# Performance work log

Hardware: AMD Instinct MI355X
Metric: run time of the kernel (lower is better)

The kernel has to match this reference:

```python
import jax, jax.numpy as jnp
import numpy as np

WIN = (2, 4, 4)
SHIFT = (1, 2, 2)
NUM_HEADS = 8
LN_EPS = 1e-5


def _rel_pos_index(ws):
    wt, wh, ww = ws
    coords = np.stack(np.meshgrid(np.arange(wt), np.arange(wh), np.arange(ww), indexing='ij'))
    cf = coords.reshape(3, -1)                      # [3, N]
    rel = cf[:, :, None] - cf[:, None, :]           # [3, N, N]
    rel = rel.transpose(1, 2, 0).copy()             # [N, N, 3]
    rel[..., 0] += wt - 1
    rel[..., 1] += wh - 1
    rel[..., 2] += ww - 1
    rel[..., 0] *= (2 * wh - 1) * (2 * ww - 1)
    rel[..., 1] *= 2 * ww - 1
    return rel.sum(-1)                              # [N, N] int

REL_IDX = _rel_pos_index(WIN)


def _layer_norm(x, w, b):
    mu = jnp.mean(x, axis=-1, keepdims=True)
    var = jnp.mean(jnp.square(x - mu), axis=-1, keepdims=True)
    return (x - mu) * jax.lax.rsqrt(var + LN_EPS) * w + b


def setup_inputs() -> dict:
    key = jax.random.key(0)
    ks = jax.random.split(key, 8)
    C, Cm = 256, 1024
    inp = {
        'x': jax.random.normal(ks[0], (2, 16, 64, 64, C), jnp.float32),
        'norm1_w': jnp.ones((C,), jnp.float32),
        'norm1_b': jnp.zeros((C,), jnp.float32),
        'qkv_w': jax.random.normal(ks[1], (C, 3 * C), jnp.float32) * 0.02,
        'qkv_b': jnp.zeros((3 * C,), jnp.float32),
        'proj_w': jax.random.normal(ks[2], (C, C), jnp.float32) * 0.02,
        'proj_b': jnp.zeros((C,), jnp.float32),
        'rel_bias_table': jax.random.normal(ks[3], (147, NUM_HEADS), jnp.float32) * 0.02,
        'norm2_w': jnp.ones((C,), jnp.float32),
        'norm2_b': jnp.zeros((C,), jnp.float32),
        'mlp_w1': jax.random.normal(ks[4], (C, Cm), jnp.float32) * 0.02,
        'mlp_b1': jnp.zeros((Cm,), jnp.float32),
        'mlp_w2': jax.random.normal(ks[5], (Cm, C), jnp.float32) * 0.02,
        'mlp_b2': jnp.zeros((C,), jnp.float32),
    }
    return inp


def reference(x, norm1_w, norm1_b, qkv_w, qkv_b, proj_w, proj_b,
              rel_bias_table, norm2_w, norm2_b, mlp_w1, mlp_b1, mlp_w2, mlp_b2):
    B, T, H, W, C = x.shape
    wT, wH, wW = WIN
    nh = NUM_HEADS
    d = C // nh
    scale = d ** (-0.5)
    N = wT * wH * wW

    shortcut = x
    h = _layer_norm(x, norm1_w, norm1_b)
    # cyclic shift (no attention mask is applied in the original block)
    h = jnp.roll(h, shift=(-SHIFT[0], -SHIFT[1], -SHIFT[2]), axis=(1, 2, 3))
    # window partition -> [B*nW, N, C]
    h = h.reshape(B, T // wT, wT, H // wH, wH, W // wW, wW, C)
    h = h.transpose(0, 1, 3, 5, 2, 4, 6, 7).reshape(-1, N, C)
    B_ = h.shape[0]

    qkv = (h @ qkv_w + qkv_b).reshape(B_, N, 3, nh, d).transpose(2, 0, 3, 1, 4)
    q, k, v = qkv[0] * scale, qkv[1], qkv[2]          # [B_, nh, N, d]
    attn = jnp.einsum('bhnd,bhmd->bhnm', q, k)        # [B_, nh, N, N]
    bias = rel_bias_table[REL_IDX].transpose(2, 0, 1)  # [nh, N, N]
    attn = jax.nn.softmax(attn + bias[None], axis=-1)
    o = jnp.einsum('bhnm,bhmd->bhnd', attn, v)
    o = o.transpose(0, 2, 1, 3).reshape(B_, N, C)
    o = o @ proj_w + proj_b

    # window reverse -> [B, T, H, W, C]
    o = o.reshape(B, T // wT, H // wH, W // wW, wT, wH, wW, C)
    o = o.transpose(0, 1, 4, 2, 5, 3, 6, 7).reshape(B, T, H, W, C)
    o = jnp.roll(o, shift=SHIFT, axis=(1, 2, 3))

    x = shortcut + o
    m = _layer_norm(x, norm2_w, norm2_b)
    m = jax.nn.gelu(m @ mlp_w1 + mlp_b1, approximate=False) @ mlp_w2 + mlp_b2
    return x + m
```

## Files before the change

kernel.cpp:

```cpp
#include <hip/hip_runtime.h>
#include <hip/hip_bf16.h>
#include <cstdint>
#include <cstddef>

typedef __attribute__((ext_vector_type(8)))  short  s16x8;
typedef __attribute__((ext_vector_type(4)))  float  fp32x4;
typedef __attribute__((ext_vector_type(16))) float  fp32x16;
typedef __attribute__((ext_vector_type(4)))  unsigned short u16x4;

static __device__ __forceinline__ float bf2f(unsigned short u) {
    union { unsigned int i; float f; } v; v.i = ((unsigned int)u) << 16; return v.f;
}
static __device__ __forceinline__ unsigned short f2bf(float f) {
    __hip_bfloat16 h = __float2bfloat16(f);
    return __builtin_bit_cast(unsigned short, h);
}

static __device__ __forceinline__ fp32x16 mfma32(s16x8 a, s16x8 b, fp32x16 c) {
    return __builtin_amdgcn_mfma_f32_32x32x16_bf16(a, b, c, 0, 0, 0);
}
static __device__ __forceinline__ fp32x4 mfma16(s16x8 a, s16x8 b, fp32x4 c) {
    return __builtin_amdgcn_mfma_f32_16x16x32_bf16(a, b, c, 0, 0, 0);
}

static __device__ __forceinline__ float wave_sum(float v) {
#pragma unroll
    for (int off = 32; off > 0; off >>= 1) v += __shfl_xor(v, off, 64);
    return v;
}

#define NTOK   131072
#define CDIM   256

__global__ void prep_kernel(const float* __restrict__ qkv_w, const float* __restrict__ proj_w,
                            const float* __restrict__ w1,    const float* __restrict__ w2,
                            const float* __restrict__ rel,
                            unsigned short* __restrict__ qkvT, unsigned short* __restrict__ projT,
                            unsigned short* __restrict__ w1T,  unsigned short* __restrict__ w2T,
                            float* __restrict__ btab) {
    int id = blockIdx.x * 256 + threadIdx.x;
    if (id < 196608) {
        int n = id >> 8, k = id & 255;
        qkvT[id] = f2bf(qkv_w[k * 768 + n]);
    } else if (id < 262144) {
        int e = id - 196608; int n = e >> 8, k = e & 255;
        projT[e] = f2bf(proj_w[k * 256 + n]);
    } else if (id < 524288) {
        int e = id - 262144; int n = e >> 8, k = e & 255;
        w1T[e] = f2bf(w1[k * 1024 + n]);
    } else if (id < 786432) {
        int e = id - 524288; int n = e >> 10, k = e & 1023;
        w2T[e] = f2bf(w2[k * 256 + n]);
    } else {
        int e = id - 786432;
        int h = e >> 10, rem = e & 1023, n = rem >> 5, m = rem & 31;
        int tn = n >> 4, hn = (n >> 2) & 3, wn = n & 3;
        int tm = m >> 4, hm = (m >> 2) & 3, wm = m & 3;
        int ridx = (tn - tm + 1) * 49 + (hn - hm + 3) * 7 + (wn - wm + 3);
        btab[e] = rel[ridx * 8 + h];
    }
}

template <int MODE>
__global__ __launch_bounds__(256) void ln_kernel(const float* __restrict__ in,
                                                 const float* __restrict__ w,
                                                 const float* __restrict__ b,
                                                 unsigned short* __restrict__ out) {
    int tid = threadIdx.x, lane = tid & 63, wid = tid >> 6;
    long r = (long)blockIdx.x * 4 + wid;
    long src;
    if (MODE == 0) {
        int n = (int)(r & 31); int win = (int)(r >> 5);
        int b_ = win >> 11, tw = (win >> 8) & 7, hw = (win >> 4) & 15, ww = win & 15;
        int ti = n >> 4, hi = (n >> 2) & 3, wi = n & 3;
        int t = tw * 2 + ti, hh = hw * 4 + hi, wv = ww * 4 + wi;
        int ts = (t + 1) & 15, hs = (hh + 2) & 63, wsd = (wv + 2) & 63;
        src = ((long)((b_ * 16 + ts) * 64 + hs)) * 64 + wsd;
    } else {
        src = r;
    }
    float4 v = *(const float4*)&in[src * CDIM + lane * 4];
    float vv[4] = {v.x, v.y, v.z, v.w};
    float s = vv[0] + vv[1] + vv[2] + vv[3];
    s = wave_sum(s);
    float mean = s * (1.0f / 256.0f);
    float q = vv[0]*vv[0] + vv[1]*vv[1] + vv[2]*vv[2] + vv[3]*vv[3];
    q = wave_sum(q);
    float var = q * (1.0f / 256.0f) - mean * mean;
    float rstd = rsqrtf(var + 1e-5f);
    int c0 = lane * 4;
    u16x4 o;
#pragma unroll
    for (int j = 0; j < 4; ++j)
        o[j] = f2bf((vv[j] - mean) * rstd * w[c0 + j] + b[c0 + j]);
    *(u16x4*)&out[r * CDIM + c0] = o;
}

template <int K, int EPI, int NS>
__global__ __launch_bounds__(256, 2) void gemm_k(const unsigned short* __restrict__ A,
                                                 const unsigned short* __restrict__ Bt,
                                                 const float* __restrict__ bias,
                                                 float* __restrict__ outf,
                                                 unsigned short* __restrict__ outb,
                                                 const float* __restrict__ resid) {
    __shared__ unsigned short smem[32768];
    const int tid = threadIdx.x;
    const int lane = tid & 63, wid = tid >> 6;
    const int m0 = blockIdx.y * 128, n0 = blockIdx.x * 128;
    const int wm = (wid >> 1) * 64, wn = (wid & 1) * 64;
    constexpr int NK = K / 64;

    fp32x4 acc[4][4] = {};

    auto stage = [&](int kt, int buf) {
#pragma unroll
        for (int i = 0; i < 4; ++i) {
            int L = i * 256 + tid;
            int r = L >> 3, c = L & 7;
            int sw = c ^ (r & 7);
            const unsigned short* ga = A + (size_t)(m0 + r) * K + kt * 64 + sw * 8;
            __builtin_amdgcn_global_load_lds(
                (const __attribute__((address_space(1))) void*)ga,
                (__attribute__((address_space(3))) void*)(smem + buf * 16384 + L * 8),
                16, 0, 0);
            const unsigned short* gb = Bt + (size_t)(n0 + r) * K + kt * 64 + sw * 8;
            __builtin_amdgcn_global_load_lds(
                (const __attribute__((address_space(1))) void*)gb,
                (__attribute__((address_space(3))) void*)(smem + buf * 16384 + 8192 + L * 8),
                16, 0, 0);
        }
    };

    stage(0, 0);
    for (int kt = 0; kt < NK; ++kt) {
        __syncthreads();
        if (kt + 1 < NK) stage(kt + 1, (kt + 1) & 1);
        const unsigned short* As = smem + (kt & 1) * 16384;
        const unsigned short* Bs = As + 8192;
#pragma unroll
        for (int ks = 0; ks < 2; ++ks) {
            s16x8 a[4], b[4];
#pragma unroll
            for (int m = 0; m < 4; ++m) {
                int row = wm + m * 16 + (lane & 15);
                int ch = (ks * 4 + (lane >> 4)) ^ (row & 7);
                a[m] = *(const s16x8*)(As + row * 64 + ch * 8);
            }
#pragma unroll
            for (int n = 0; n < 4; ++n) {
                int row = wn + n * 16 + (lane & 15);
                int ch = (ks * 4 + (lane >> 4)) ^ (row & 7);
                b[n] = *(const s16x8*)(Bs + row * 64 + ch * 8);
            }
#pragma unroll
            for (int m = 0; m < 4; ++m)
#pragma unroll
                for (int n = 0; n < 4; ++n)
                    acc[m][n] = mfma16(a[m], b[n], acc[m][n]);
        }
    }

    float bv[4];
#pragma unroll
    for (int n = 0; n < 4; ++n) bv[n] = bias[n0 + wn + n * 16 + (lane & 15)];

#pragma unroll
    for (int m = 0; m < 4; ++m) {
#pragma unroll
        for (int rg = 0; rg < 4; ++rg) {
            int row_t = wm + m * 16 + ((lane >> 4) << 2) + rg;
            size_t gr = (size_t)m0 + row_t;
            size_t dst = 0;
            if (EPI == 1) {
                int win = (int)(gr >> 5), n_ = (int)(gr & 31);
                int b_ = win >> 11, tw = (win >> 8) & 7, hw = (win >> 4) & 15, ww = win & 15;
                int ti = n_ >> 4, hi = (n_ >> 2) & 3, wi = n_ & 3;
                int t = tw * 2 + ti, hh = hw * 4 + hi, wv = ww * 4 + wi;
                int ts = (t + 1) & 15, hs = (hh + 2) & 63, wsd = (wv + 2) & 63;
                dst = ((size_t)((b_ * 16 + ts) * 64 + hs)) * 64 + wsd;
            }
#pragma unroll
            for (int n = 0; n < 4; ++n) {
                int gc = n0 + wn + n * 16 + (lane & 15);
                float v = acc[m][n][rg] + bv[n];
                if (EPI == 0) {
                    outb[gr * NS + gc] = f2bf(v);
                } else if (EPI == 1) {
                    outf[dst * CDIM + gc] = resid[dst * CDIM + gc] + v;
                } else if (EPI == 2) {
                    float g = 0.5f * v * (1.0f + erff(v * 0.70710678118654752f));
                    outb[gr * NS + gc] = f2bf(g);
                } else {
                    outf[gr * NS + gc] += v;
                }
            }
        }
    }
}

__global__ __launch_bounds__(256) void attn_kernel(const unsigned short* __restrict__ qkv,
                                                   const float* __restrict__ btab,
                                                   unsigned short* __restrict__ obuf) {
    __shared__ unsigned short sP[4][1280];
    __shared__ unsigned short sVt[4][1280];
    int tid = threadIdx.x, lane = tid & 63, wid = tid >> 6;
    int task = blockIdx.x * 4 + wid;
    int win = task >> 3, hh = task & 7;
    const unsigned short* base = qkv + (size_t)win * 32 * 768 + hh * 32;
    int q = lane & 31, h = lane >> 5;

    s16x8 v0 = *(const s16x8*)(base + 512 + q * 768 + h * 16);
    s16x8 v1 = *(const s16x8*)(base + 512 + q * 768 + h * 16 + 8);
#pragma unroll
    for (int j = 0; j < 8; ++j) {
        sVt[wid][(h * 16 + j) * 40 + q]     = (unsigned short)v0[j];
        sVt[wid][(h * 16 + 8 + j) * 40 + q] = (unsigned short)v1[j];
    }

    s16x8 aq0 = *(const s16x8*)(base + q * 768 + h * 8);
    s16x8 aq1 = *(const s16x8*)(base + q * 768 + 16 + h * 8);
    s16x8 bk0 = *(const s16x8*)(base + 256 + q * 768 + h * 8);
    s16x8 bk1 = *(const s16x8*)(base + 256 + q * 768 + 16 + h * 8);
    fp32x16 S = {0.0f};
    S = mfma32(aq0, bk0, S);
    S = mfma32(aq1, bk1, S);

    const float scale = 0.17677669529663687f;
    float pr[16];
#pragma unroll
    for (int r = 0; r < 16; ++r) {
        int row = (r & 3) + 8 * (r >> 2) + 4 * h;
        float bvv = btab[(hh * 32 + row) * 32 + q];
        pr[r] = S[r] * scale + bvv;
    }
#pragma unroll
    for (int r = 0; r < 16; ++r) {
        float mx = pr[r];
#pragma unroll
        for (int off = 16; off > 0; off >>= 1) mx = fmaxf(mx, __shfl_xor(mx, off, 64));
        float e = __expf(pr[r] - mx);
        float sm = e;
#pragma unroll
        for (int off = 16; off > 0; off >>= 1) sm += __shfl_xor(sm, off, 64);
        pr[r] = e * __builtin_amdgcn_rcpf(sm);
    }
#pragma unroll
    for (int r = 0; r < 16; ++r) {
        int row = (r & 3) + 8 * (r >> 2) + 4 * h;
        sP[wid][row * 40 + q] = f2bf(pr[r]);
    }
    __syncthreads();

    s16x8 pa0 = *(const s16x8*)&sP[wid][q * 40 + h * 8];
    s16x8 pa1 = *(const s16x8*)&sP[wid][q * 40 + 16 + h * 8];
    s16x8 vb0 = *(const s16x8*)&sVt[wid][q * 40 + h * 8];
    s16x8 vb1 = *(const s16x8*)&sVt[wid][q * 40 + 16 + h * 8];
    fp32x16 O = {0.0f};
    O = mfma32(pa0, vb0, O);
    O = mfma32(pa1, vb1, O);
#pragma unroll
    for (int r = 0; r < 16; ++r) {
        int row = (r & 3) + 8 * (r >> 2) + 4 * h;
        obuf[((size_t)win * 32 + row) * 256 + hh * 32 + q] = f2bf(O[r]);
    }
}

extern "C" void kernel_launch(void* const* d_in, const int* in_sizes, int n_in,
                              void* d_out, int out_size, void* d_ws, size_t ws_size,
                              hipStream_t stream) {
    const float* x      = (const float*)d_in[0];
    const float* n1w    = (const float*)d_in[1];
    const float* n1b    = (const float*)d_in[2];
    const float* qkv_w  = (const float*)d_in[3];
    const float* qkv_b  = (const float*)d_in[4];
    const float* proj_w = (const float*)d_in[5];
    const float* proj_b = (const float*)d_in[6];
    const float* rel    = (const float*)d_in[7];
    const float* n2w    = (const float*)d_in[8];
    const float* n2b    = (const float*)d_in[9];
    const float* w1     = (const float*)d_in[10];
    const float* b1     = (const float*)d_in[11];
    const float* w2     = (const float*)d_in[12];
    const float* b2     = (const float*)d_in[13];
    float* out = (float*)d_out;

    char* ws = (char*)d_ws;
    unsigned short* hwin = (unsigned short*)ws;
    unsigned short* big  = (unsigned short*)(ws + 67108864);
    char* wreg = ws + 67108864 + 268435456;
    unsigned short* qkvT  = (unsigned short*)(wreg);
    unsigned short* projT = (unsigned short*)(wreg + 393216);
    unsigned short* w1T   = (unsigned short*)(wreg + 524288);
    unsigned short* w2T   = (unsigned short*)(wreg + 1048576);
    float*          btab  = (float*)(wreg + 1572864);

    prep_kernel<<<3104, 256, 0, stream>>>(qkv_w, proj_w, w1, w2, rel, qkvT, projT, w1T, w2T, btab);

    ln_kernel<0><<<NTOK / 4, 256, 0, stream>>>(x, n1w, n1b, hwin);

    gemm_k<256, 0, 768><<<dim3(6, 1024), 256, 0, stream>>>(hwin, qkvT, qkv_b, nullptr, big, nullptr);

    attn_kernel<<<8192, 256, 0, stream>>>(big, btab, hwin);

    gemm_k<256, 1, 256><<<dim3(2, 1024), 256, 0, stream>>>(hwin, projT, proj_b, out, nullptr, x);

    ln_kernel<1><<<NTOK / 4, 256, 0, stream>>>(out, n2w, n2b, hwin);

    gemm_k<256, 2, 1024><<<dim3(8, 1024), 256, 0, stream>>>(hwin, w1T, b1, nullptr, big, nullptr);

    gemm_k<1024, 3, 256><<<dim3(2, 1024), 256, 0, stream>>>(big, w2T, b2, out, nullptr, nullptr);
}
```

Before: 599.3 us.

## Enlarge GEMM tiles to 256x256 with 512 threads and XCD-aware block mapping

Replaces the 128x128, 256-thread GEMM kernel with a 256x256, 512-thread version. Each wave now holds an 8x4 grid of accumulators, computed in four sub-quadrants. The launch grid becomes 1D, and block IDs are remapped so consecutive tiles are spread across the 8 XCDs. The goal is more operand reuse per LDS load and better L2 locality for all four GEMMs. In exchange, the kernel needs 128KB of dynamic LDS and more registers per wave, which limits occupancy to about one block per CU and leaves fewer blocks for tail balance.

```diff
diff --git a/kernel.cpp b/kernel.cpp
--- a/kernel.cpp
+++ b/kernel.cpp
@@ -96,80 +96,94 @@
     *(u16x4*)&out[r * CDIM + c0] = o;
 }
 
-template <int K, int EPI, int NS>
-__global__ __launch_bounds__(256, 2) void gemm_k(const unsigned short* __restrict__ A,
-                                                 const unsigned short* __restrict__ Bt,
-                                                 const float* __restrict__ bias,
-                                                 float* __restrict__ outf,
-                                                 unsigned short* __restrict__ outb,
-                                                 const float* __restrict__ resid) {
-    __shared__ unsigned short smem[32768];
+template <int K, int EPI, int NS, int NX>
+__global__ __launch_bounds__(512) void gemm256(const unsigned short* __restrict__ A,
+                                               const unsigned short* __restrict__ Bt,
+                                               const float* __restrict__ bias,
+                                               float* __restrict__ outf,
+                                               unsigned short* __restrict__ outb,
+                                               const float* __restrict__ resid) {
+    extern __shared__ unsigned short lds[];
     const int tid = threadIdx.x;
     const int lane = tid & 63, wid = tid >> 6;
-    const int m0 = blockIdx.y * 128, n0 = blockIdx.x * 128;
-    const int wm = (wid >> 1) * 64, wn = (wid & 1) * 64;
+    const int wm = wid >> 2, wn = wid & 3;
+    constexpr int NWG = NX * 512;
+    constexpr int CPX = NWG / 8;
+    const int bid = blockIdx.x;
+    const int wg = (bid & 7) * CPX + (bid >> 3);
+    const int n0 = (wg % NX) * 256;
+    const size_t m0 = (size_t)(wg / NX) * 256;
     constexpr int NK = K / 64;
 
-    fp32x4 acc[4][4] = {};
+    fp32x4 acc[8][4] = {};
 
     auto stage = [&](int kt, int buf) {
 #pragma unroll
         for (int i = 0; i < 4; ++i) {
-            int L = i * 256 + tid;
+            int L = i * 512 + tid;
             int r = L >> 3, c = L & 7;
-            int sw = c ^ (r & 7);
-            const unsigned short* ga = A + (size_t)(m0 + r) * K + kt * 64 + sw * 8;
+            int sc = c ^ (r & 7);
+            const unsigned short* ga = A + (m0 + r) * K + kt * 64 + sc * 8;
             __builtin_amdgcn_global_load_lds(
                 (const __attribute__((address_space(1))) void*)ga,
-                (__attribute__((address_space(3))) void*)(smem + buf * 16384 + L * 8),
+                (__attribute__((address_space(3))) void*)(lds + buf * 16384 + L * 8),
                 16, 0, 0);
-            const unsigned short* gb = Bt + (size_t)(n0 + r) * K + kt * 64 + sw * 8;
+            const unsigned short* gb = Bt + (size_t)(n0 + r) * K + kt * 64 + sc * 8;
             __builtin_amdgcn_global_load_lds(
                 (const __attribute__((address_space(1))) void*)gb,
-                (__attribute__((address_space(3))) void*)(smem + buf * 16384 + 8192 + L * 8),
+                (__attribute__((address_space(3))) void*)(lds + 32768 + buf * 16384 + L * 8),
                 16, 0, 0);
         }
     };
 
     stage(0, 0);
+    __syncthreads();
     for (int kt = 0; kt < NK; ++kt) {
+        if (kt + 1 < NK) stage(kt + 1, (kt + 1) & 1);
+        const unsigned short* As = lds + (kt & 1) * 16384;
+        const unsigned short* Bs = lds + 32768 + (kt & 1) * 16384;
+#pragma unroll
+        for (int q = 0; q < 4; ++q) {
+            const int qm = q >> 1, qn = q & 1;
+            s16x8 a[4][2], b[2][2];
+#pragma unroll
+            for (int m = 0; m < 4; ++m)
+#pragma unroll
+                for (int ks = 0; ks < 2; ++ks) {
+                    int row = wm * 128 + qm * 64 + m * 16 + (lane & 15);
+                    int j = ks * 4 + (lane >> 4);
+                    a[m][ks] = *(const s16x8*)(As + row * 64 + ((j ^ (row & 7)) << 3));
+                }
+#pragma unroll
+            for (int n = 0; n < 2; ++n)
+#pragma unroll
+                for (int ks = 0; ks < 2; ++ks) {
+                    int row = wn * 64 + qn * 32 + n * 16 + (lane & 15);
+                    int j = ks * 4 + (lane >> 4);
+                    b[n][ks] = *(const s16x8*)(Bs + row * 64 + ((j ^ (row & 7)) << 3));
+                }
+#pragma unroll
+            for (int ks = 0; ks < 2; ++ks)
+#pragma unroll
+                for (int m = 0; m < 4; ++m)
+#pragma unroll
+                    for (int n = 0; n < 2; ++n)
+                        acc[qm * 4 + m][qn * 2 + n] =
+                            mfma16(a[m][ks], b[n][ks], acc[qm * 4 + m][qn * 2 + n]);
+        }
         __syncthreads();
-        if (kt + 1 < NK) stage(kt + 1, (kt + 1) & 1);
-        const unsigned short* As = smem + (kt & 1) * 16384;
-        const unsigned short* Bs = As + 8192;
-#pragma unroll
-        for (int ks = 0; ks < 2; ++ks) {
-            s16x8 a[4], b[4];
-#pragma unroll
-            for (int m = 0; m < 4; ++m) {
-                int row = wm + m * 16 + (lane & 15);
-                int ch = (ks * 4 + (lane >> 4)) ^ (row & 7);
-                a[m] = *(const s16x8*)(As + row * 64 + ch * 8);
-            }
-#pragma unroll
-            for (int n = 0; n < 4; ++n) {
-                int row = wn + n * 16 + (lane & 15);
-                int ch = (ks * 4 + (lane >> 4)) ^ (row & 7);
-                b[n] = *(const s16x8*)(Bs + row * 64 + ch * 8);
-            }
-#pragma unroll
-            for (int m = 0; m < 4; ++m)
-#pragma unroll
-                for (int n = 0; n < 4; ++n)
-                    acc[m][n] = mfma16(a[m], b[n], acc[m][n]);
-        }
     }
 
     float bv[4];
 #pragma unroll
-    for (int n = 0; n < 4; ++n) bv[n] = bias[n0 + wn + n * 16 + (lane & 15)];
-
-#pragma unroll
-    for (int m = 0; m < 4; ++m) {
+    for (int n = 0; n < 4; ++n) bv[n] = bias[n0 + wn * 64 + n * 16 + (lane & 15)];
+
+#pragma unroll
+    for (int m = 0; m < 8; ++m) {
 #pragma unroll
         for (int rg = 0; rg < 4; ++rg) {
-            int row_t = wm + m * 16 + ((lane >> 4) << 2) + rg;
-            size_t gr = (size_t)m0 + row_t;
+            int row_t = wm * 128 + m * 16 + ((lane >> 4) << 2) + rg;
+            size_t gr = m0 + row_t;
             size_t dst = 0;
             if (EPI == 1) {
                 int win = (int)(gr >> 5), n_ = (int)(gr & 31);
@@ -181,7 +195,7 @@
             }
 #pragma unroll
             for (int n = 0; n < 4; ++n) {
-                int gc = n0 + wn + n * 16 + (lane & 15);
+                int gc = n0 + wn * 64 + n * 16 + (lane & 15);
                 float v = acc[m][n][rg] + bv[n];
                 if (EPI == 0) {
                     outb[gr * NS + gc] = f2bf(v);
@@ -298,15 +312,15 @@
 
     ln_kernel<0><<<NTOK / 4, 256, 0, stream>>>(x, n1w, n1b, hwin);
 
-    gemm_k<256, 0, 768><<<dim3(6, 1024), 256, 0, stream>>>(hwin, qkvT, qkv_b, nullptr, big, nullptr);
+    gemm256<256, 0, 768, 3><<<1536, 512, 131072, stream>>>(hwin, qkvT, qkv_b, nullptr, big, nullptr);
 
     attn_kernel<<<8192, 256, 0, stream>>>(big, btab, hwin);
 
-    gemm_k<256, 1, 256><<<dim3(2, 1024), 256, 0, stream>>>(hwin, projT, proj_b, out, nullptr, x);
+    gemm256<256, 1, 256, 1><<<512, 512, 131072, stream>>>(hwin, projT, proj_b, out, nullptr, x);
 
     ln_kernel<1><<<NTOK / 4, 256, 0, stream>>>(out, n2w, n2b, hwin);
 
-    gemm_k<256, 2, 1024><<<dim3(8, 1024), 256, 0, stream>>>(hwin, w1T, b1, nullptr, big, nullptr);
-
-    gemm_k<1024, 3, 256><<<dim3(2, 1024), 256, 0, stream>>>(big, w2T, b2, out, nullptr, nullptr);
-}
+    gemm256<256, 2, 1024, 4><<<2048, 512, 131072, stream>>>(hwin, w1T, b1, nullptr, big, nullptr);
+
+    gemm256<1024, 3, 256, 1><<<512, 512, 131072, stream>>>(big, w2T, b2, out, nullptr, nullptr);
+}
```

Result: no change. 597.8 us (-0.3%).
